# Kernel tuning notes

Measured on AMD Instinct MI355X. Metric: run time of the kernel, lower is better.

## Reference

```python
import jax, jax.numpy as jnp
import numpy as np

N_NODES = 100000
N_EDGES = 1600000
IN_FEATS = 128
HEADS = 4
OUT_FEATS = 16


def setup_inputs() -> dict:
    key = jax.random.key(0)
    k1, k2, k3, k4, k5 = jax.random.split(key, 5)
    x = jax.random.normal(k1, (N_NODES, IN_FEATS), dtype=jnp.float32)
    edge_index = jax.random.randint(k2, (2, N_EDGES), 0, N_NODES, dtype=jnp.int64)
    # glorot init scales
    s_w = float(np.sqrt(6.0 / (IN_FEATS + HEADS * OUT_FEATS)))
    s_a = float(np.sqrt(6.0 / (HEADS + OUT_FEATS)))
    W = jax.random.uniform(k3, (HEADS * OUT_FEATS, IN_FEATS), jnp.float32, -s_w, s_w)
    att_i = jax.random.uniform(k4, (1, HEADS, OUT_FEATS), jnp.float32, -s_a, s_a)
    att_j = jax.random.uniform(k5, (1, HEADS, OUT_FEATS), jnp.float32, -s_a, s_a)
    return {"x": x, "edge_index": edge_index, "W": W, "att_i": att_i, "att_j": att_j}


def reference(x, edge_index, W, att_i, att_j):
    N = x.shape[0]
    H, F = att_i.shape[1], att_i.shape[2]
    src = edge_index[0]  # j (source / message sender)
    dst = edge_index[1]  # i (destination / softmax segment)
    # linear projection: [N, H, F]
    h = (x @ W.T).reshape(N, H, F)
    h_j = h[src]  # [E, H, F]
    h_i = h[dst]  # [E, H, F]
    # attention logits per edge per head
    alpha = jnp.einsum('ehf,khf->eh', h_i, att_i) + jnp.einsum('ehf,khf->eh', h_j, att_j)
    alpha = jax.nn.leaky_relu(alpha, negative_slope=0.01)
    # segment softmax over incoming edges of each destination node
    amax = jax.ops.segment_max(alpha, dst, num_segments=N)  # [N, H]
    amax = jnp.where(jnp.isfinite(amax), amax, 0.0)
    ex = jnp.exp(alpha - amax[dst])
    denom = jax.ops.segment_sum(ex, dst, num_segments=N)  # [N, H]
    alpha = ex / (denom[dst] + 1e-16)
    # weighted scatter-sum aggregation
    msg = h_j * alpha[:, :, None]  # [E, H, F]
    out = jax.ops.segment_sum(msg, dst, num_segments=N)  # [N, H, F]
    return out.reshape(N, H * F)
```

## Files before the change

kernel.cpp:

```cpp
#include <hip/hip_runtime.h>

typedef __attribute__((ext_vector_type(8))) short short8;
typedef __attribute__((ext_vector_type(4))) float f32x4;

#define N_NODES 100000
#define N_EDGES 1600000
#define IN_F 128
#define OUT_ALL 64
#define HEADS 4
#define OUT_F 16
#define NTILES (N_NODES / 16)
#define BIN_BLOCKS 250
#define EPB (N_EDGES / BIN_BLOCKS)
#define TOTAL_BLOCKS 2048
#define PROJ_BLOCKS (TOTAL_BLOCKS - BIN_BLOCKS)
#define SLICE_SHIFT 8
#define SLICE_NODES 256
#define NSLICES ((N_NODES + SLICE_NODES - 1) / SLICE_NODES)
#define SEG_CAP 4608
#define QUARTER_NODES 64
#define SORT_CAP 1280

static __device__ __forceinline__ ushort f2bf(float f) {
    unsigned u = __float_as_uint(f);
    return (ushort)((u + 0x7FFF + ((u >> 16) & 1)) >> 16);
}
static __device__ __forceinline__ float bf2f(ushort b) {
    return __uint_as_float(((unsigned)b) << 16);
}
static __device__ __forceinline__ float lrelu(float v) {
    return v > 0.f ? v : 0.01f * v;
}
static __device__ __forceinline__ short8 pack_bf16x8(float4 f0, float4 f1) {
    union { unsigned u[4]; short8 s; } r;
    asm("v_cvt_pk_bf16_f32 %0, %1, %2" : "=v"(r.u[0]) : "v"(f0.x), "v"(f0.y));
    asm("v_cvt_pk_bf16_f32 %0, %1, %2" : "=v"(r.u[1]) : "v"(f0.z), "v"(f0.w));
    asm("v_cvt_pk_bf16_f32 %0, %1, %2" : "=v"(r.u[2]) : "v"(f1.x), "v"(f1.y));
    asm("v_cvt_pk_bf16_f32 %0, %1, %2" : "=v"(r.u[3]) : "v"(f1.z), "v"(f1.w));
    return r.s;
}

__global__ __launch_bounds__(256) void prep_kernel(
    const float* __restrict__ W, const float* __restrict__ att_i,
    const float* __restrict__ att_j, float* __restrict__ wiwj,
    int* __restrict__ scursor)
{
    int idx = blockIdx.x * 256 + threadIdx.x;
    if (idx < NSLICES) scursor[idx] = 0;
    if (idx >= IN_F * 8) return;
    int k = idx >> 3, c = idx & 7;
    int h = c & 3;
    const float* att = (c < 4) ? att_i : att_j;
    float s = 0.f;
    #pragma unroll
    for (int f = 0; f < 16; ++f)
        s += W[(size_t)(h * 16 + f) * IN_F + k] * att[h * OUT_F + f];
    wiwj[k * 8 + c] = s;
}

__global__ __launch_bounds__(256) void proj_bin_kernel(
    const float* __restrict__ x, const float* __restrict__ W,
    const float* __restrict__ wiwj, const int* __restrict__ ei,
    ushort* __restrict__ hb, float* __restrict__ ai, float* __restrict__ aj,
    int* __restrict__ scursor, int2* __restrict__ seg)
{
    __shared__ int cnt[NSLICES];
    __shared__ int gbase[NSLICES];
    __shared__ int run[NSLICES];
    __shared__ __align__(16) ushort xsb[16][144];

    if (blockIdx.x < BIN_BLOCKS) {
        int base = blockIdx.x * EPB;
        const int4* __restrict__ srcp = (const int4*)(ei + base);
        const int4* __restrict__ dstp = (const int4*)(ei + N_EDGES + base);
        for (int s = threadIdx.x; s < NSLICES; s += 256) { cnt[s] = 0; run[s] = 0; }
        __syncthreads();
        for (int i = threadIdx.x; i < EPB / 4; i += 256) {
            int4 d = dstp[i];
            atomicAdd(&cnt[d.x >> SLICE_SHIFT], 1);
            atomicAdd(&cnt[d.y >> SLICE_SHIFT], 1);
            atomicAdd(&cnt[d.z >> SLICE_SHIFT], 1);
            atomicAdd(&cnt[d.w >> SLICE_SHIFT], 1);
        }
        __syncthreads();
        for (int s = threadIdx.x; s < NSLICES; s += 256) {
            int c = cnt[s];
            gbase[s] = c ? atomicAdd(&scursor[s], c) : 0;
        }
        __syncthreads();
        for (int i = threadIdx.x; i < EPB / 4; i += 256) {
            int4 sv = srcp[i];
            int4 dv = dstp[i];
            int ss, p;
            ss = dv.x >> SLICE_SHIFT; p = gbase[ss] + atomicAdd(&run[ss], 1);
            if (p < SEG_CAP) seg[(size_t)ss * SEG_CAP + p] = make_int2(sv.x, dv.x);
            ss = dv.y >> SLICE_SHIFT; p = gbase[ss] + atomicAdd(&run[ss], 1);
            if (p < SEG_CAP) seg[(size_t)ss * SEG_CAP + p] = make_int2(sv.y, dv.y);
            ss = dv.z >> SLICE_SHIFT; p = gbase[ss] + atomicAdd(&run[ss], 1);
            if (p < SEG_CAP) seg[(size_t)ss * SEG_CAP + p] = make_int2(sv.z, dv.z);
            ss = dv.w >> SLICE_SHIFT; p = gbase[ss] + atomicAdd(&run[ss], 1);
            if (p < SEG_CAP) seg[(size_t)ss * SEG_CAP + p] = make_int2(sv.w, dv.w);
        }
        return;
    }

    int bproj = blockIdx.x - BIN_BLOCKS;
    const int nproj = PROJ_BLOCKS;

    int w   = threadIdx.x >> 6;
    int l   = threadIdx.x & 63;
    int col = l & 15;
    int kg  = l >> 4;

    short8 bw[4];
    #pragma unroll
    for (int m = 0; m < 4; ++m) {
        const float* wp = W + (size_t)(w * 16 + col) * IN_F + m * 32 + kg * 8;
        float4 f0 = *(const float4*)wp;
        float4 f1 = *(const float4*)(wp + 4);
        bw[m] = pack_bf16x8(f0, f1);
    }
    short8 bwd[4];
    #pragma unroll
    for (int m = 0; m < 4; ++m) {
        float v[8];
        #pragma unroll
        for (int j = 0; j < 8; ++j)
            v[j] = (col < 8) ? wiwj[(size_t)(m * 32 + kg * 8 + j) * 8 + col] : 0.f;
        bwd[m] = pack_bf16x8(float4{v[0], v[1], v[2], v[3]},
                             float4{v[4], v[5], v[6], v[7]});
    }

    int srow = threadIdx.x >> 4;
    int sc8  = threadIdx.x & 15;

    float4 p0 = {0,0,0,0}, p1 = {0,0,0,0};
    if (bproj < NTILES) {
        const float* xp = x + (size_t)(bproj * 16 + srow) * IN_F + sc8 * 8;
        p0 = *(const float4*)xp;
        p1 = *(const float4*)(xp + 4);
    }

    for (int t = bproj; t < NTILES; t += nproj) {
        int nodeBase = t * 16;

        __syncthreads();
        *(short8*)&xsb[srow][sc8 * 8] = pack_bf16x8(p0, p1);
        __syncthreads();

        short8 a[4];
        #pragma unroll
        for (int m = 0; m < 4; ++m)
            a[m] = *(const short8*)&xsb[col][m * 32 + kg * 8];

        int tn = t + nproj;
        if (tn < NTILES) {
            const float* xp = x + (size_t)(tn * 16 + srow) * IN_F + sc8 * 8;
            p0 = *(const float4*)xp;
            p1 = *(const float4*)(xp + 4);
        }

        f32x4 acc = {0.f, 0.f, 0.f, 0.f};
        f32x4 accd = {0.f, 0.f, 0.f, 0.f};
        #pragma unroll
        for (int m = 0; m < 4; ++m) {
            acc  = __builtin_amdgcn_mfma_f32_16x16x32_bf16(a[m], bw[m],  acc,  0, 0, 0);
            accd = __builtin_amdgcn_mfma_f32_16x16x32_bf16(a[m], bwd[m], accd, 0, 0, 0);
        }

        #pragma unroll
        for (int r = 0; r < 4; ++r)
            hb[(size_t)(nodeBase + kg * 4 + r) * OUT_ALL + w * 16 + col] = f2bf(acc[r]);

        if (col < 4) {
            #pragma unroll
            for (int r = 0; r < 4; ++r)
                ai[(size_t)(nodeBase + kg * 4 + r) * HEADS + col] = accd[r];
        } else if (col < 8) {
            #pragma unroll
            for (int r = 0; r < 4; ++r)
                aj[(size_t)(nodeBase + kg * 4 + r) * HEADS + (col - 4)] = accd[r];
        }
    }
}

__global__ __launch_bounds__(512) void agg_kernel(
    const int2* __restrict__ seg, const int* __restrict__ scursor,
    const ushort* __restrict__ hb, const float* __restrict__ ai,
    const float* __restrict__ aj, float* __restrict__ out)
{
    __shared__ int staged[SORT_CAP];
    __shared__ int sorted_src[SORT_CAP];
    __shared__ int cnt[QUARTER_NODES];
    __shared__ int run[QUARTER_NODES];
    __shared__ int rowptr[QUARTER_NODES + 1];
    __shared__ int scnt_s;

    int s       = blockIdx.x >> 2;
    int quarter = blockIdx.x & 3;
    int nbase   = (s << SLICE_SHIFT) + quarter * QUARTER_NODES;
    int total = scursor[s]; if (total > SEG_CAP) total = SEG_CAP;
    const int2* sp = seg + (size_t)s * SEG_CAP;

    for (int i = threadIdx.x; i < QUARTER_NODES; i += 512) { cnt[i] = 0; run[i] = 0; }
    if (threadIdx.x == 0) scnt_s = 0;
    __syncthreads();

    int lane = threadIdx.x & 63;
    for (int i = threadIdx.x; i < total; i += 512) {
        int2 e = sp[i];
        int d = e.y & (SLICE_NODES - 1);
        bool m = (d >> 6) == quarter;
        unsigned long long mask = __ballot(m);
        if (mask) {
            int leader = (int)__ffsll((long long)mask) - 1;
            int base = 0;
            if (lane == leader)
                base = atomicAdd(&scnt_s, (int)__popcll(mask));
            base = __shfl(base, leader, 64);
            if (m) {
                int p = base + (int)__popcll(mask & ((1ull << lane) - 1ull));
                if (p < SORT_CAP) staged[p] = (e.x << 6) | (d & 63);
                atomicAdd(&cnt[d & 63], 1);
            }
        }
    }
    __syncthreads();

    if (threadIdx.x < 64) {
        int l = threadIdx.x;
        int v = cnt[l];
        int inc = v;
        #pragma unroll
        for (int d = 1; d < 64; d <<= 1) {
            int t = __shfl_up(inc, d, 64);
            if (l >= d) inc += t;
        }
        rowptr[l] = inc - v;
        if (l == 63) rowptr[64] = inc;
    }
    __syncthreads();

    int scnt = scnt_s; if (scnt > SORT_CAP) scnt = SORT_CAP;
    for (int i = threadIdx.x; i < scnt; i += 512) {
        int v = staged[i];
        int lb = v & 63;
        int p = rowptr[lb] + atomicAdd(&run[lb], 1);
        if (p < SORT_CAP) sorted_src[p] = (int)((unsigned)v >> 6);
    }
    __syncthreads();

    int g    = threadIdx.x >> 3;
    int sub  = threadIdx.x & 7;
    int head = sub >> 1;
    int node = nbase + g;
    if (node >= N_NODES) return;
    int beg = rowptr[g], end = rowptr[g + 1];
    if (end > SORT_CAP) end = SORT_CAP;
    float aiv = ai[(size_t)node * HEADS + head];
    float acc[8] = {0.f, 0.f, 0.f, 0.f, 0.f, 0.f, 0.f, 0.f};
    float den = 0.f;

    int k = beg;
    for (; k + 4 <= end; k += 4) {
        int s0 = sorted_src[k + 0];
        int s1 = sorted_src[k + 1];
        int s2 = sorted_src[k + 2];
        int s3 = sorted_src[k + 3];
        float aj0 = aj[(size_t)s0 * HEADS + head];
        float aj1 = aj[(size_t)s1 * HEADS + head];
        float aj2 = aj[(size_t)s2 * HEADS + head];
        float aj3 = aj[(size_t)s3 * HEADS + head];
        short8 h0 = *(const short8*)(hb + (size_t)s0 * OUT_ALL + sub * 8);
        short8 h1 = *(const short8*)(hb + (size_t)s1 * OUT_ALL + sub * 8);
        short8 h2 = *(const short8*)(hb + (size_t)s2 * OUT_ALL + sub * 8);
        short8 h3 = *(const short8*)(hb + (size_t)s3 * OUT_ALL + sub * 8);
        float e0 = __expf(lrelu(aiv + aj0));
        float e1 = __expf(lrelu(aiv + aj1));
        float e2 = __expf(lrelu(aiv + aj2));
        float e3 = __expf(lrelu(aiv + aj3));
        den += (e0 + e1) + (e2 + e3);
        #pragma unroll
        for (int q = 0; q < 8; ++q)
            acc[q] += e0 * bf2f((ushort)h0[q]) + e1 * bf2f((ushort)h1[q]) +
                      e2 * bf2f((ushort)h2[q]) + e3 * bf2f((ushort)h3[q]);
    }
    for (; k < end; ++k) {
        int src = sorted_src[k];
        float ex = __expf(lrelu(aiv + aj[(size_t)src * HEADS + head]));
        den += ex;
        short8 hv = *(const short8*)(hb + (size_t)src * OUT_ALL + sub * 8);
        #pragma unroll
        for (int q = 0; q < 8; ++q)
            acc[q] += ex * bf2f((ushort)hv[q]);
    }

    float inv = 1.0f / (den + 1e-16f);
    float4 o0 = {acc[0] * inv, acc[1] * inv, acc[2] * inv, acc[3] * inv};
    float4 o1 = {acc[4] * inv, acc[5] * inv, acc[6] * inv, acc[7] * inv};
    float* op = out + (size_t)node * OUT_ALL + sub * 8;
    *(float4*)op = o0;
    *(float4*)(op + 4) = o1;
}

extern "C" void kernel_launch(void* const* d_in, const int* in_sizes, int n_in,
                              void* d_out, int out_size, void* d_ws, size_t ws_size,
                              hipStream_t stream) {
    const float* x     = (const float*)d_in[0];
    const int*   ei    = (const int*)d_in[1];
    const float* W     = (const float*)d_in[2];
    const float* att_i = (const float*)d_in[3];
    const float* att_j = (const float*)d_in[4];
    float* out = (float*)d_out;

    char* ws = (char*)d_ws;
    size_t off = 0;
    auto alloc = [&](size_t bytes) {
        void* p = ws + off;
        off += (bytes + 255) & ~(size_t)255;
        return p;
    };
    ushort* hb      = (ushort*)alloc((size_t)N_NODES * OUT_ALL * 2);
    float*  ai      = (float*)alloc((size_t)N_NODES * HEADS * 4);
    float*  aj      = (float*)alloc((size_t)N_NODES * HEADS * 4);
    float*  wiwj    = (float*)alloc((size_t)IN_F * 8 * 4);
    int*    scursor = (int*)alloc((size_t)NSLICES * 4);
    int2*   seg     = (int2*)alloc((size_t)NSLICES * SEG_CAP * 8);

    prep_kernel<<<(IN_F * 8 + 255) / 256, 256, 0, stream>>>(
        W, att_i, att_j, wiwj, scursor);
    proj_bin_kernel<<<TOTAL_BLOCKS, 256, 0, stream>>>(
        x, W, wiwj, ei, hb, ai, aj, scursor, seg);
    agg_kernel<<<NSLICES * 4, 512, 0, stream>>>(seg, scursor, hb, ai, aj, out);
}
```

Measured before the change: 89.39 us.

## Pack binned edges into 32-bit words and remap agg block order

```diff
diff --git a/kernel.cpp b/kernel.cpp
--- a/kernel.cpp
+++ b/kernel.cpp
@@ -20,6 +20,7 @@
 #define SEG_CAP 4608
 #define QUARTER_NODES 64
 #define SORT_CAP 1280
+#define AGG_GRID 1568
 
 static __device__ __forceinline__ ushort f2bf(float f) {
     unsigned u = __float_as_uint(f);
@@ -62,7 +63,7 @@
     const float* __restrict__ x, const float* __restrict__ W,
     const float* __restrict__ wiwj, const int* __restrict__ ei,
     ushort* __restrict__ hb, float* __restrict__ ai, float* __restrict__ aj,
-    int* __restrict__ scursor, int2* __restrict__ seg)
+    int* __restrict__ scursor, int* __restrict__ seg)
 {
     __shared__ int cnt[NSLICES];
     __shared__ int gbase[NSLICES];
@@ -93,13 +94,13 @@
             int4 dv = dstp[i];
             int ss, p;
             ss = dv.x >> SLICE_SHIFT; p = gbase[ss] + atomicAdd(&run[ss], 1);
-            if (p < SEG_CAP) seg[(size_t)ss * SEG_CAP + p] = make_int2(sv.x, dv.x);
+            if (p < SEG_CAP) seg[(size_t)ss * SEG_CAP + p] = (sv.x << 8) | (dv.x & 255);
             ss = dv.y >> SLICE_SHIFT; p = gbase[ss] + atomicAdd(&run[ss], 1);
-            if (p < SEG_CAP) seg[(size_t)ss * SEG_CAP + p] = make_int2(sv.y, dv.y);
+            if (p < SEG_CAP) seg[(size_t)ss * SEG_CAP + p] = (sv.y << 8) | (dv.y & 255);
             ss = dv.z >> SLICE_SHIFT; p = gbase[ss] + atomicAdd(&run[ss], 1);
-            if (p < SEG_CAP) seg[(size_t)ss * SEG_CAP + p] = make_int2(sv.z, dv.z);
+            if (p < SEG_CAP) seg[(size_t)ss * SEG_CAP + p] = (sv.z << 8) | (dv.z & 255);
             ss = dv.w >> SLICE_SHIFT; p = gbase[ss] + atomicAdd(&run[ss], 1);
-            if (p < SEG_CAP) seg[(size_t)ss * SEG_CAP + p] = make_int2(sv.w, dv.w);
+            if (p < SEG_CAP) seg[(size_t)ss * SEG_CAP + p] = (sv.w << 8) | (dv.w & 255);
         }
         return;
     }
@@ -185,7 +186,7 @@
 }
 
 __global__ __launch_bounds__(512) void agg_kernel(
-    const int2* __restrict__ seg, const int* __restrict__ scursor,
+    const int* __restrict__ seg, const int* __restrict__ scursor,
     const ushort* __restrict__ hb, const float* __restrict__ ai,
     const float* __restrict__ aj, float* __restrict__ out)
 {
@@ -196,11 +197,13 @@
     __shared__ int rowptr[QUARTER_NODES + 1];
     __shared__ int scnt_s;
 
-    int s       = blockIdx.x >> 2;
-    int quarter = blockIdx.x & 3;
+    int b = blockIdx.x;
+    int s = (b & 7) + 8 * ((b >> 3) >> 2);
+    if (s >= NSLICES) return;
+    int quarter = (b >> 3) & 3;
     int nbase   = (s << SLICE_SHIFT) + quarter * QUARTER_NODES;
     int total = scursor[s]; if (total > SEG_CAP) total = SEG_CAP;
-    const int2* sp = seg + (size_t)s * SEG_CAP;
+    const int* sp = seg + (size_t)s * SEG_CAP;
 
     for (int i = threadIdx.x; i < QUARTER_NODES; i += 512) { cnt[i] = 0; run[i] = 0; }
     if (threadIdx.x == 0) scnt_s = 0;
@@ -208,8 +211,8 @@
 
     int lane = threadIdx.x & 63;
     for (int i = threadIdx.x; i < total; i += 512) {
-        int2 e = sp[i];
-        int d = e.y & (SLICE_NODES - 1);
+        int e = sp[i];
+        int d = e & 255;
         bool m = (d >> 6) == quarter;
         unsigned long long mask = __ballot(m);
         if (mask) {
@@ -220,7 +223,7 @@
             base = __shfl(base, leader, 64);
             if (m) {
                 int p = base + (int)__popcll(mask & ((1ull << lane) - 1ull));
-                if (p < SORT_CAP) staged[p] = (e.x << 6) | (d & 63);
+                if (p < SORT_CAP) staged[p] = (((unsigned)e >> 8) << 6) | (d & 63);
                 atomicAdd(&cnt[d & 63], 1);
             }
         }
@@ -325,11 +328,11 @@
     float*  aj      = (float*)alloc((size_t)N_NODES * HEADS * 4);
     float*  wiwj    = (float*)alloc((size_t)IN_F * 8 * 4);
     int*    scursor = (int*)alloc((size_t)NSLICES * 4);
-    int2*   seg     = (int2*)alloc((size_t)NSLICES * SEG_CAP * 8);
+    int*    seg     = (int*)alloc((size_t)NSLICES * SEG_CAP * 4);
 
     prep_kernel<<<(IN_F * 8 + 255) / 256, 256, 0, stream>>>(
         W, att_i, att_j, wiwj, scursor);
     proj_bin_kernel<<<TOTAL_BLOCKS, 256, 0, stream>>>(
         x, W, wiwj, ei, hb, ai, aj, scursor, seg);
-    agg_kernel<<<NSLICES * 4, 512, 0, stream>>>(seg, scursor, hb, ai, aj, out);
-}
+    agg_kernel<<<AGG_GRID, 512, 0, stream>>>(seg, scursor, hb, ai, aj, out);
+}
```

Result: faster. 86.50 us (median of 2 runs) (-3.2%).
